# Performance work log

Hardware: AMD Instinct MI355X
Metric: run time of the kernel (lower is better)

## Reference

```python
import jax, jax.numpy as jnp
import numpy as np

NUM_ITER = 2
B, NS, NK = 64, 11, 4096
QI = KVI = QKO = VO = 128
LN_EPS = 1e-5
ATTN_EPS = 1e-8


def setup_inputs() -> dict:
    key = jax.random.key(0)
    ks = jax.random.split(key, 20)
    rn = lambda i, shp, sc: jax.random.normal(ks[i], shp, jnp.float32) * sc
    d = {
        "query": rn(0, (B, NS, QI), 1.0),
        "inputs": rn(1, (B, NK, KVI), 1.0),
        # LayerNorm params
        "ln_q_g": jnp.ones((QI,), jnp.float32),
        "ln_q_b": jnp.zeros((QI,), jnp.float32),
        "ln_kv_g": jnp.ones((KVI,), jnp.float32),
        "ln_kv_b": jnp.zeros((KVI,), jnp.float32),
        # projections (stored [in, out]; torch Linear weight transposed)
        "Wq": rn(2, (QI, QKO), QI ** -0.5),
        "Wk": rn(3, (KVI, QKO), KVI ** -0.5),
        "Wv": rn(4, (KVI, VO), KVI ** -0.5),
        # GRU cell params
        "W_ir": rn(5, (VO, VO), VO ** -0.5),
        "b_ir": jnp.zeros((VO,), jnp.float32),
        "W_iz": rn(6, (VO, VO), VO ** -0.5),
        "b_iz": jnp.zeros((VO,), jnp.float32),
        "W_hr": rn(7, (VO, VO), VO ** -0.5),
        "W_hz": rn(8, (VO, VO), VO ** -0.5),
        "W_in": rn(9, (VO, VO), VO ** -0.5),
        "b_in": jnp.zeros((VO,), jnp.float32),
        "W_hn": rn(10, (VO, VO), VO ** -0.5),
        "b_hn": jnp.zeros((VO,), jnp.float32),
    }
    return d


def _layernorm(x, g, b):
    mu = x.mean(-1, keepdims=True)
    var = ((x - mu) ** 2).mean(-1, keepdims=True)  # biased var, matches torch LN
    return (x - mu) * jax.lax.rsqrt(var + LN_EPS) * g + b


def reference(query, inputs, ln_q_g, ln_q_b, ln_kv_g, ln_kv_b, Wq, Wk, Wv,
              W_ir, b_ir, W_iz, b_iz, W_hr, W_hz, W_in, b_in, W_hn, b_hn):
    x = _layernorm(inputs, ln_kv_g, ln_kv_b)          # [b, nk, kvi]
    k = x @ Wk                                        # [b, nk, qko]
    v = x @ Wv                                        # [b, nk, vo]
    scale = 1.0 / jnp.sqrt(jnp.float32(Wq.shape[1]))
    for _ in range(NUM_ITER):
        q = _layernorm(query, ln_q_g, ln_q_b) @ Wq    # [b, ns, qko]
        q = q * scale
        # inverted SDPA: softmax over slot axis m, renormalize over key axis n
        a = jax.nn.softmax(jnp.einsum('bmc,bnc->bmn', q, k), axis=1)
        a = a / (a.sum(axis=2, keepdims=True) + ATTN_EPS)
        upd = jnp.einsum('bmn,bnc->bmc', a, v)        # [b, ns, vo]
        # GRU cell update (per-slot)
        r = jax.nn.sigmoid(upd @ W_ir + b_ir + query @ W_hr)
        z = jax.nn.sigmoid(upd @ W_iz + b_iz + query @ W_hz)
        n = jnp.tanh(upd @ W_in + b_in + r * (query @ W_hn + b_hn))
        query = (1.0 - z) * n + z * query
    return query
```

## Files before the change

kernel.cpp:

```cpp
#include <hip/hip_runtime.h>
#include <hip/hip_bf16.h>


#define NKEYS 4096

typedef short short8 __attribute__((ext_vector_type(8)));
typedef float f32x4 __attribute__((ext_vector_type(4)));

__device__ __forceinline__ unsigned short f2bf(float x) {
    unsigned u = __float_as_uint(x);
    u += 0x7fffu + ((u >> 16) & 1u);
    return (unsigned short)(u >> 16);
}

__device__ __forceinline__ int xoff(int n, int cb) {
    return n * 256 + (cb ^ ((n & 7) << 4) ^ (((n >> 3) & 3) << 5));
}

__device__ __forceinline__ void gll16(const void* g, void* l) {
    __builtin_amdgcn_global_load_lds(
        (const __attribute__((address_space(1))) unsigned int*)g,
        (__attribute__((address_space(3))) unsigned int*)l, 16, 0, 0);
}

__global__ void kqq(const float* __restrict__ query, const float* __restrict__ g,
                    const float* __restrict__ be, const float* __restrict__ Wq,
                    const float* __restrict__ Wk, char* __restrict__ qfrag) {
    int bm = blockIdx.x;
    int b = bm / 11, m = bm - b * 11;
    int c = threadIdx.x;
    __shared__ float xs[128], qs[128];
    __shared__ float red[4];
    float x = query[bm * 128 + c];
    float s = x, ss = x * x;
#pragma unroll
    for (int mask = 1; mask < 64; mask <<= 1) {
        s += __shfl_xor(s, mask);
        ss += __shfl_xor(ss, mask);
    }
    int wid = threadIdx.x >> 6;
    if ((threadIdx.x & 63) == 0) { red[wid] = s; red[2 + wid] = ss; }
    __syncthreads();
    s = red[0] + red[1]; ss = red[2] + red[3];
    float mean = s * (1.f / 128.f);
    float var = ss * (1.f / 128.f) - mean * mean;
    float rstd = rsqrtf(var + 1e-5f);
    xs[c] = (x - mean) * rstd * g[c] + be[c];
    __syncthreads();
    float acc = 0.f;
#pragma unroll 8
    for (int k = 0; k < 128; k++) acc += xs[k] * Wq[k * 128 + c];
    qs[c] = acc * 0.088388347648318447f;
    __syncthreads();
    const float4* wr = (const float4*)(Wk + c * 128);
    float qk = 0.f;
#pragma unroll 8
    for (int k4 = 0; k4 < 32; k4++) {
        float4 wv = wr[k4];
        qk += qs[k4 * 4] * wv.x + qs[k4 * 4 + 1] * wv.y +
              qs[k4 * 4 + 2] * wv.z + qs[k4 * 4 + 3] * wv.w;
    }
    int kc = c >> 5, hi = (c >> 3) & 3, j = c & 7;
    *(unsigned short*)(qfrag + b * 4096 + kc * 1024 + (hi * 16 + m) * 16 + j * 2) = f2bf(qk);
}

__global__ __launch_bounds__(256) void kf(
    const float* __restrict__ inputs, const float* __restrict__ gkv,
    const float* __restrict__ bkv, const char* __restrict__ qfrag,
    char* __restrict__ kg, float* __restrict__ yacc, float* __restrict__ dacc_g) {
    __shared__ __align__(16) char smem[18432];
    const int PO = 16384;
    int tid = threadIdx.x;
    int b = blockIdx.x >> 4, gt = blockIdx.x & 15;
    int w = tid >> 6, lane = tid & 63, hi = lane >> 4, lo = lane & 15;
    int a_ = tid >> 5, col4 = tid & 31;

    short8 qa[4];
#pragma unroll
    for (int kc = 0; kc < 4; kc++)
        qa[kc] = *(const short8*)(qfrag + b * 4096 + kc * 1024 + lane * 16);

    float4 g4  = *(const float4*)(gkv + col4 * 4);
    float4 be4 = *(const float4*)(bkv + col4 * 4);

    f32x4 y0 = {0, 0, 0, 0}, y1 = {0, 0, 0, 0};
    float dr[4] = {0, 0, 0, 0};

    const float4* inp4 = (const float4*)(inputs + ((size_t)b * NKEYS + gt * 256) * 128);

    float4 xa[8];
#pragma unroll
    for (int i = 0; i < 8; i++) xa[i] = inp4[tid + 256 * i];

#pragma unroll
    for (int t = 0; t < 4; t++) {
        float4 xb[8];
        if (t < 3) {
#pragma unroll
            for (int i = 0; i < 8; i++) xb[i] = inp4[(t + 1) * 2048 + tid + 256 * i];
        }
        size_t tb = ((size_t)(b * 64 + gt * 4 + t)) * 16384;
#pragma unroll
        for (int i = 0; i < 8; i++) {
            float4 xv = xa[i];
            int row = a_ + 8 * i;
            float s = xv.x + xv.y + xv.z + xv.w;
            float ss = xv.x * xv.x + xv.y * xv.y + xv.z * xv.z + xv.w * xv.w;
#pragma unroll
            for (int mask = 1; mask < 32; mask <<= 1) {
                s += __shfl_xor(s, mask);
                ss += __shfl_xor(ss, mask);
            }
            float mean = s * (1.f / 128.f);
            float var = ss * (1.f / 128.f) - mean * mean;
            float rstd = rsqrtf(var + 1e-5f);
            unsigned short h0 = f2bf((xv.x - mean) * rstd * g4.x + be4.x);
            unsigned short h1 = f2bf((xv.y - mean) * rstd * g4.y + be4.y);
            unsigned short h2 = f2bf((xv.z - mean) * rstd * g4.z + be4.z);
            unsigned short h3 = f2bf((xv.w - mean) * rstd * g4.w + be4.w);
            uint2 pk;
            pk.x = (unsigned)h0 | ((unsigned)h1 << 16);
            pk.y = (unsigned)h2 | ((unsigned)h3 << 16);
            int off = xoff(row, col4 * 8);
            *(uint2*)(smem + off) = pk;
            *(uint2*)(kg + tb + off) = pk;
        }
        asm volatile("s_waitcnt lgkmcnt(0)" ::: "memory");
        __builtin_amdgcn_s_barrier();
        __builtin_amdgcn_sched_barrier(0);

        f32x4 lacc = {0, 0, 0, 0};
        int n = w * 16 + lo;
#pragma unroll
        for (int kc = 0; kc < 4; kc++) {
            short8 kf8 = *(short8*)(smem + xoff(n, kc * 64 + hi * 16));
            lacc = __builtin_amdgcn_mfma_f32_16x16x32_bf16(qa[kc], kf8, lacc, 0, 0, 0);
        }
        float mx = -1e30f;
#pragma unroll
        for (int r = 0; r < 4; r++) {
            int m = hi * 4 + r;
            mx = fmaxf(mx, (m < 11) ? lacc[r] : -1e30f);
        }
        mx = fmaxf(mx, __shfl_xor(mx, 16));
        mx = fmaxf(mx, __shfl_xor(mx, 32));
        float p[4]; float s = 0.f;
#pragma unroll
        for (int r = 0; r < 4; r++) {
            int m = hi * 4 + r;
            p[r] = (m < 11) ? __expf(lacc[r] - mx) : 0.f;
            s += p[r];
        }
        s += __shfl_xor(s, 16);
        s += __shfl_xor(s, 32);
        float inv = 1.f / s;
#pragma unroll
        for (int r = 0; r < 4; r++) {
            p[r] *= inv;
            dr[r] += p[r];
            int m = hi * 4 + r;
            *(unsigned short*)(smem + PO + m * 128 + (((w * 16 + lo) * 2) ^ ((m & 7) << 4))) =
                f2bf(p[r]);
        }
        asm volatile("s_waitcnt lgkmcnt(0)" ::: "memory");
        __builtin_amdgcn_s_barrier();
        __builtin_amdgcn_sched_barrier(0);

#pragma unroll
        for (int s2 = 0; s2 < 2; s2++) {
            short8 pf = *(short8*)(smem + PO + lo * 128 + ((s2 * 64 + hi * 16) ^ ((lo & 7) << 4)));
            short8 v0, v1;
#pragma unroll
            for (int j = 0; j < 8; j++) {
                int nn = s2 * 32 + hi * 8 + j;
                v0[j] = *(short*)(smem + xoff(nn, (w * 32 + lo) * 2));
                v1[j] = *(short*)(smem + xoff(nn, (w * 32 + 16 + lo) * 2));
            }
            y0 = __builtin_amdgcn_mfma_f32_16x16x32_bf16(pf, v0, y0, 0, 0, 0);
            y1 = __builtin_amdgcn_mfma_f32_16x16x32_bf16(pf, v1, y1, 0, 0, 0);
        }
        asm volatile("s_waitcnt lgkmcnt(0)" ::: "memory");
        __builtin_amdgcn_s_barrier();
        __builtin_amdgcn_sched_barrier(0);
        if (t < 3) {
#pragma unroll
            for (int i = 0; i < 8; i++) xa[i] = xb[i];
        }
    }

#pragma unroll
    for (int r = 0; r < 4; r++) {
        int m = hi * 4 + r;
        if (m < 11) {
            atomicAdd(&yacc[(b * 16 + m) * 128 + w * 32 + lo], y0[r]);
            atomicAdd(&yacc[(b * 16 + m) * 128 + w * 32 + 16 + lo], y1[r]);
        }
    }
#pragma unroll
    for (int mask = 1; mask < 16; mask <<= 1) {
#pragma unroll
        for (int r = 0; r < 4; r++) dr[r] += __shfl_xor(dr[r], mask);
    }
    if (lo == 0) {
#pragma unroll
        for (int r = 0; r < 4; r++) {
            int m = hi * 4 + r;
            if (m < 11) atomicAdd(&dacc_g[b * 16 + m], dr[r]);
        }
    }
}

__global__ __launch_bounds__(256) void kb(
    const char* __restrict__ kg, const char* __restrict__ qfrag,
    float* __restrict__ yacc, float* __restrict__ dacc_g) {
    __shared__ __align__(16) char smem[34816];
    const int PO = 32768;
    int tid = threadIdx.x;
    int b = blockIdx.x >> 4, gt = blockIdx.x & 15;
    int w = tid >> 6, lane = tid & 63, hi = lane >> 4, lo = lane & 15;

    short8 qa[4];
#pragma unroll
    for (int kc = 0; kc < 4; kc++)
        qa[kc] = *(const short8*)(qfrag + b * 4096 + kc * 1024 + lane * 16);

    f32x4 y0 = {0, 0, 0, 0}, y1 = {0, 0, 0, 0};
    float dr[4] = {0, 0, 0, 0};

    size_t base = ((size_t)(b * 64 + gt * 4)) * 16384;
    int reg = w * 4096;

#pragma unroll
    for (int j = 0; j < 4; j++) {
        int o = reg + j * 1024;
        gll16(kg + base + o + lane * 16, smem + o);
    }

#pragma unroll
    for (int t = 0; t < 4; t++) {
        int XB = (t & 1) * 16384;
        if (t < 3) {
            size_t tbn = base + (size_t)(t + 1) * 16384;
            int nb = ((t + 1) & 1) * 16384;
#pragma unroll
            for (int j = 0; j < 4; j++) {
                int o = reg + j * 1024;
                gll16(kg + tbn + o + lane * 16, smem + nb + o);
            }
            asm volatile("s_waitcnt vmcnt(4)" ::: "memory");
        } else {
            asm volatile("s_waitcnt vmcnt(0)" ::: "memory");
        }
        __builtin_amdgcn_s_barrier();
        __builtin_amdgcn_sched_barrier(0);

        f32x4 lacc = {0, 0, 0, 0};
        int n = w * 16 + lo;
#pragma unroll
        for (int kc = 0; kc < 4; kc++) {
            short8 kf8 = *(short8*)(smem + XB + xoff(n, kc * 64 + hi * 16));
            lacc = __builtin_amdgcn_mfma_f32_16x16x32_bf16(qa[kc], kf8, lacc, 0, 0, 0);
        }
        float mx = -1e30f;
#pragma unroll
        for (int r = 0; r < 4; r++) {
            int m = hi * 4 + r;
            mx = fmaxf(mx, (m < 11) ? lacc[r] : -1e30f);
        }
        mx = fmaxf(mx, __shfl_xor(mx, 16));
        mx = fmaxf(mx, __shfl_xor(mx, 32));
        float p[4]; float s = 0.f;
#pragma unroll
        for (int r = 0; r < 4; r++) {
            int m = hi * 4 + r;
            p[r] = (m < 11) ? __expf(lacc[r] - mx) : 0.f;
            s += p[r];
        }
        s += __shfl_xor(s, 16);
        s += __shfl_xor(s, 32);
        float inv = 1.f / s;
#pragma unroll
        for (int r = 0; r < 4; r++) {
            p[r] *= inv;
            dr[r] += p[r];
            int m = hi * 4 + r;
            *(unsigned short*)(smem + PO + m * 128 + (((w * 16 + lo) * 2) ^ ((m & 7) << 4))) =
                f2bf(p[r]);
        }
        asm volatile("s_waitcnt lgkmcnt(0)" ::: "memory");
        __builtin_amdgcn_s_barrier();
        __builtin_amdgcn_sched_barrier(0);

#pragma unroll
        for (int s2 = 0; s2 < 2; s2++) {
            short8 pf = *(short8*)(smem + PO + lo * 128 + ((s2 * 64 + hi * 16) ^ ((lo & 7) << 4)));
            short8 v0, v1;
#pragma unroll
            for (int j = 0; j < 8; j++) {
                int nn = s2 * 32 + hi * 8 + j;
                v0[j] = *(short*)(smem + XB + xoff(nn, (w * 32 + lo) * 2));
                v1[j] = *(short*)(smem + XB + xoff(nn, (w * 32 + 16 + lo) * 2));
            }
            y0 = __builtin_amdgcn_mfma_f32_16x16x32_bf16(pf, v0, y0, 0, 0, 0);
            y1 = __builtin_amdgcn_mfma_f32_16x16x32_bf16(pf, v1, y1, 0, 0, 0);
        }
        asm volatile("s_waitcnt lgkmcnt(0)" ::: "memory");
        __builtin_amdgcn_s_barrier();
        __builtin_amdgcn_sched_barrier(0);
    }

#pragma unroll
    for (int r = 0; r < 4; r++) {
        int m = hi * 4 + r;
        if (m < 11) {
            atomicAdd(&yacc[(b * 16 + m) * 128 + w * 32 + lo], y0[r]);
            atomicAdd(&yacc[(b * 16 + m) * 128 + w * 32 + 16 + lo], y1[r]);
        }
    }
#pragma unroll
    for (int mask = 1; mask < 16; mask <<= 1) {
#pragma unroll
        for (int r = 0; r < 4; r++) dr[r] += __shfl_xor(dr[r], mask);
    }
    if (lo == 0) {
#pragma unroll
        for (int r = 0; r < 4; r++) {
            int m = hi * 4 + r;
            if (m < 11) atomicAdd(&dacc_g[b * 16 + m], dr[r]);
        }
    }
}

__global__ void kun(const float* __restrict__ yacc, const float* __restrict__ dacc,
                    const float* __restrict__ qcur, const float* __restrict__ Wv,
                    const float* __restrict__ W_ir, const float* __restrict__ b_ir,
                    const float* __restrict__ W_iz, const float* __restrict__ b_iz,
                    const float* __restrict__ W_hr, const float* __restrict__ W_hz,
                    const float* __restrict__ W_in, const float* __restrict__ b_in,
                    const float* __restrict__ W_hn, const float* __restrict__ b_hn,
                    float* __restrict__ qnext) {
    int bm = blockIdx.x;
    int b = bm / 11, m = bm % 11;
    int c = threadIdx.x;
    __shared__ float ys[128], us[128], qs[128];
    float den = dacc[b * 16 + m] + 1e-8f;
    ys[c] = yacc[(b * 16 + m) * 128 + c] / den;
    qs[c] = qcur[bm * 128 + c];
    __syncthreads();
    float upd = 0.f;
#pragma unroll 4
    for (int k = 0; k < 128; k++) upd += ys[k] * Wv[k * 128 + c];
    us[c] = upd;
    __syncthreads();
    float air = 0, aiz = 0, ain = 0, ahr = 0, ahz = 0, ahn = 0;
#pragma unroll 4
    for (int k = 0; k < 128; k++) {
        float u = us[k], q = qs[k];
        air += u * W_ir[k * 128 + c];
        aiz += u * W_iz[k * 128 + c];
        ain += u * W_in[k * 128 + c];
        ahr += q * W_hr[k * 128 + c];
        ahz += q * W_hz[k * 128 + c];
        ahn += q * W_hn[k * 128 + c];
    }
    float r = 1.f / (1.f + expf(-(air + b_ir[c] + ahr)));
    float z = 1.f / (1.f + expf(-(aiz + b_iz[c] + ahz)));
    float n = tanhf(ain + b_in[c] + r * (ahn + b_hn[c]));
    qnext[bm * 128 + c] = (1.f - z) * n + z * qs[c];
}

__global__ void kq(const float* __restrict__ query, const float* __restrict__ g,
                   const float* __restrict__ be, const float* __restrict__ Wq,
                   float* __restrict__ qout) {
    int bm = blockIdx.x;
    int c = threadIdx.x;
    __shared__ float xs[128];
    __shared__ float red[4];
    float x = query[bm * 128 + c];
    float s = x, ss = x * x;
#pragma unroll
    for (int mask = 1; mask < 64; mask <<= 1) {
        s += __shfl_xor(s, mask);
        ss += __shfl_xor(ss, mask);
    }
    int wid = threadIdx.x >> 6;
    if ((threadIdx.x & 63) == 0) { red[wid] = s; red[2 + wid] = ss; }
    __syncthreads();
    s = red[0] + red[1]; ss = red[2] + red[3];
    float mean = s * (1.f / 128.f);
    float var = ss * (1.f / 128.f) - mean * mean;
    float rstd = rsqrtf(var + 1e-5f);
    xs[c] = (x - mean) * rstd * g[c] + be[c];
    __syncthreads();
    float acc = 0.f;
#pragma unroll 8
    for (int k = 0; k < 128; k++) acc += xs[k] * Wq[k * 128 + c];
    qout[bm * 128 + c] = acc * 0.088388347648318447f;
}

__global__ __launch_bounds__(256) void ks(
    const float* __restrict__ inputs, const float* __restrict__ gkv,
    const float* __restrict__ bkv, const float* __restrict__ Wk,
    const float* __restrict__ Wv, const float* __restrict__ qbuf,
    float* __restrict__ upd_acc, float* __restrict__ d_acc) {
    __shared__ __align__(16) char smem[51200];
    const int XO = 0, KO = 16384, VB = 32768, PO = 49152;

    int tid = threadIdx.x;
    int b = blockIdx.x >> 4, g = blockIdx.x & 15;
    int w = tid >> 6, lane = tid & 63, hi = lane >> 4, lo = lane & 15;

    short8 bk[2][4], bv[2][4];
#pragma unroll
    for (int ct = 0; ct < 2; ct++) {
        int col = w * 32 + ct * 16 + lo;
#pragma unroll
        for (int kc = 0; kc < 4; kc++) {
            short8 fk, fv;
#pragma unroll
            for (int j = 0; j < 8; j++) {
                int rr = kc * 32 + hi * 8 + j;
                fk[j] = (short)f2bf(Wk[rr * 128 + col]);
                fv[j] = (short)f2bf(Wv[rr * 128 + col]);
            }
            bk[ct][kc] = fk; bv[ct][kc] = fv;
        }
    }
    short8 qa[4];
#pragma unroll
    for (int kc = 0; kc < 4; kc++) {
        short8 f;
#pragma unroll
        for (int j = 0; j < 8; j++)
            f[j] = (lo < 11) ? (short)f2bf(qbuf[(b * 11 + lo) * 128 + kc * 32 + hi * 8 + j])
                             : (short)0;
        qa[kc] = f;
    }
    int col4 = tid & 31;
    float4 g4  = *(const float4*)(gkv + col4 * 4);
    float4 be4 = *(const float4*)(bkv + col4 * 4);

    f32x4 uacc0 = {0, 0, 0, 0}, uacc1 = {0, 0, 0, 0};
    float dacc[4] = {0, 0, 0, 0};

    const float4* inp4 = (const float4*)(inputs + ((size_t)b * NKEYS + g * 256) * 128);
    int a_ = tid >> 5;

    for (int t = 0; t < 4; t++) {
#pragma unroll
        for (int i = 0; i < 8; i++) {
            int f = tid + 256 * i;
            float4 xv = inp4[t * 2048 + f];
            int row = a_ + 8 * i;
            float s = xv.x + xv.y + xv.z + xv.w;
            float ss = xv.x * xv.x + xv.y * xv.y + xv.z * xv.z + xv.w * xv.w;
#pragma unroll
            for (int mask = 1; mask < 32; mask <<= 1) {
                s += __shfl_xor(s, mask);
                ss += __shfl_xor(ss, mask);
            }
            float mean = s * (1.f / 128.f);
            float var = ss * (1.f / 128.f) - mean * mean;
            float rstd = rsqrtf(var + 1e-5f);
            unsigned short h0 = f2bf((xv.x - mean) * rstd * g4.x + be4.x);
            unsigned short h1 = f2bf((xv.y - mean) * rstd * g4.y + be4.y);
            unsigned short h2 = f2bf((xv.z - mean) * rstd * g4.z + be4.z);
            unsigned short h3 = f2bf((xv.w - mean) * rstd * g4.w + be4.w);
            uint2 pk;
            pk.x = (unsigned)h0 | ((unsigned)h1 << 16);
            pk.y = (unsigned)h2 | ((unsigned)h3 << 16);
            int byte = row * 256 + ((col4 * 8) ^ ((row & 7) << 4));
            *(uint2*)(smem + XO + byte) = pk;
        }
        __syncthreads();
#pragma unroll
        for (int mt = 0; mt < 4; mt++) {
            f32x4 ka0 = {0,0,0,0}, ka1 = {0,0,0,0}, va0 = {0,0,0,0}, va1 = {0,0,0,0};
            int arow = mt * 16 + lo;
#pragma unroll
            for (int kc = 0; kc < 4; kc++) {
                int abyte = arow * 256 + ((kc * 64 + hi * 16) ^ ((arow & 7) << 4));
                short8 af = *(short8*)(smem + XO + abyte);
                ka0 = __builtin_amdgcn_mfma_f32_16x16x32_bf16(af, bk[0][kc], ka0, 0, 0, 0);
                ka1 = __builtin_amdgcn_mfma_f32_16x16x32_bf16(af, bk[1][kc], ka1, 0, 0, 0);
                va0 = __builtin_amdgcn_mfma_f32_16x16x32_bf16(af, bv[0][kc], va0, 0, 0, 0);
                va1 = __builtin_amdgcn_mfma_f32_16x16x32_bf16(af, bv[1][kc], va1, 0, 0, 0);
            }
#pragma unroll
            for (int r = 0; r < 4; r++) {
                int n = mt * 16 + hi * 4 + r;
                int c0 = w * 32 + lo;
                int c1 = c0 + 16;
                *(unsigned short*)(smem + KO + n * 256 + ((c0 * 2) ^ ((n & 7) << 4))) = f2bf(ka0[r]);
                *(unsigned short*)(smem + KO + n * 256 + ((c1 * 2) ^ ((n & 7) << 4))) = f2bf(ka1[r]);
                *(unsigned short*)(smem + VB + c0 * 128 + ((n * 2) ^ ((c0 & 7) << 4))) = f2bf(va0[r]);
                *(unsigned short*)(smem + VB + c1 * 128 + ((n * 2) ^ ((c1 & 7) << 4))) = f2bf(va1[r]);
            }
        }
        __syncthreads();
        {
            f32x4 lacc = {0, 0, 0, 0};
            int n = w * 16 + lo;
#pragma unroll
            for (int kc = 0; kc < 4; kc++) {
                int kbyte = n * 256 + ((kc * 64 + hi * 16) ^ ((n & 7) << 4));
                short8 kf8 = *(short8*)(smem + KO + kbyte);
                lacc = __builtin_amdgcn_mfma_f32_16x16x32_bf16(qa[kc], kf8, lacc, 0, 0, 0);
            }
            float mx = -1e30f;
#pragma unroll
            for (int r = 0; r < 4; r++) {
                int m = hi * 4 + r;
                float v = (m < 11) ? lacc[r] : -1e30f;
                mx = fmaxf(mx, v);
            }
            mx = fmaxf(mx, __shfl_xor(mx, 16));
            mx = fmaxf(mx, __shfl_xor(mx, 32));
            float p[4]; float s = 0.f;
#pragma unroll
            for (int r = 0; r < 4; r++) {
                int m = hi * 4 + r;
                p[r] = (m < 11) ? __expf(lacc[r] - mx) : 0.f;
                s += p[r];
            }
            s += __shfl_xor(s, 16);
            s += __shfl_xor(s, 32);
            float inv = 1.f / s;
#pragma unroll
            for (int r = 0; r < 4; r++) {
                p[r] *= inv;
                dacc[r] += p[r];
                int m = hi * 4 + r;
                *(unsigned short*)(smem + PO + m * 128 + (((w * 16 + lo) * 2) ^ ((m & 7) << 4))) =
                    f2bf(p[r]);
            }
        }
        __syncthreads();
#pragma unroll
        for (int kc2 = 0; kc2 < 2; kc2++) {
            int pbyte = lo * 128 + ((kc2 * 64 + hi * 16) ^ ((lo & 7) << 4));
            short8 pf = *(short8*)(smem + PO + pbyte);
            int c0 = w * 32 + lo;
            int vb0 = c0 * 128 + ((kc2 * 64 + hi * 16) ^ ((c0 & 7) << 4));
            short8 vf0 = *(short8*)(smem + VB + vb0);
            uacc0 = __builtin_amdgcn_mfma_f32_16x16x32_bf16(pf, vf0, uacc0, 0, 0, 0);
            int c1 = c0 + 16;
            int vb1 = c1 * 128 + ((kc2 * 64 + hi * 16) ^ ((c1 & 7) << 4));
            short8 vf1 = *(short8*)(smem + VB + vb1);
            uacc1 = __builtin_amdgcn_mfma_f32_16x16x32_bf16(pf, vf1, uacc1, 0, 0, 0);
        }
    }
#pragma unroll
    for (int r = 0; r < 4; r++) {
        int m = hi * 4 + r;
        if (m < 11) {
            atomicAdd(&upd_acc[(b * 16 + m) * 128 + w * 32 + lo], uacc0[r]);
            atomicAdd(&upd_acc[(b * 16 + m) * 128 + w * 32 + 16 + lo], uacc1[r]);
        }
    }
#pragma unroll
    for (int mask = 1; mask < 16; mask <<= 1) {
#pragma unroll
        for (int r = 0; r < 4; r++) dacc[r] += __shfl_xor(dacc[r], mask);
    }
    if (lo == 0) {
#pragma unroll
        for (int r = 0; r < 4; r++) {
            int m = hi * 4 + r;
            if (m < 11) atomicAdd(&d_acc[b * 16 + m], dacc[r]);
        }
    }
}

__global__ void ku(const float* __restrict__ upd_acc, const float* __restrict__ d_acc,
                   const float* __restrict__ qcur,
                   const float* __restrict__ W_ir, const float* __restrict__ b_ir,
                   const float* __restrict__ W_iz, const float* __restrict__ b_iz,
                   const float* __restrict__ W_hr, const float* __restrict__ W_hz,
                   const float* __restrict__ W_in, const float* __restrict__ b_in,
                   const float* __restrict__ W_hn, const float* __restrict__ b_hn,
                   float* __restrict__ qnext) {
    int bm = blockIdx.x;
    int b = bm / 11, m = bm % 11;
    int c = threadIdx.x;
    __shared__ float us[128], qs[128];
    float den = d_acc[b * 16 + m] + 1e-8f;
    us[c] = upd_acc[(b * 16 + m) * 128 + c] / den;
    qs[c] = qcur[bm * 128 + c];
    __syncthreads();
    float air = 0, aiz = 0, ain = 0, ahr = 0, ahz = 0, ahn = 0;
#pragma unroll 4
    for (int k = 0; k < 128; k++) {
        float u = us[k], q = qs[k];
        air += u * W_ir[k * 128 + c];
        aiz += u * W_iz[k * 128 + c];
        ain += u * W_in[k * 128 + c];
        ahr += q * W_hr[k * 128 + c];
        ahz += q * W_hz[k * 128 + c];
        ahn += q * W_hn[k * 128 + c];
    }
    float r = 1.f / (1.f + expf(-(air + b_ir[c] + ahr)));
    float z = 1.f / (1.f + expf(-(aiz + b_iz[c] + ahz)));
    float n = tanhf(ain + b_in[c] + r * (ahn + b_hn[c]));
    qnext[bm * 128 + c] = (1.f - z) * n + z * qs[c];
}

extern "C" void kernel_launch(void* const* d_in, const int* in_sizes, int n_in,
                              void* d_out, int out_size, void* d_ws, size_t ws_size,
                              hipStream_t stream) {
    const float* query   = (const float*)d_in[0];
    const float* inputs  = (const float*)d_in[1];
    const float* ln_q_g  = (const float*)d_in[2];
    const float* ln_q_b  = (const float*)d_in[3];
    const float* ln_kv_g = (const float*)d_in[4];
    const float* ln_kv_b = (const float*)d_in[5];
    const float* Wq      = (const float*)d_in[6];
    const float* Wk      = (const float*)d_in[7];
    const float* Wv      = (const float*)d_in[8];
    const float* W_ir    = (const float*)d_in[9];
    const float* b_ir    = (const float*)d_in[10];
    const float* W_iz    = (const float*)d_in[11];
    const float* b_iz    = (const float*)d_in[12];
    const float* W_hr    = (const float*)d_in[13];
    const float* W_hz    = (const float*)d_in[14];
    const float* W_in    = (const float*)d_in[15];
    const float* b_in    = (const float*)d_in[16];
    const float* W_hn    = (const float*)d_in[17];
    const float* b_hn    = (const float*)d_in[18];

    char* ws = (char*)d_ws;
    float* query_buf = (float*)(ws);
    float* yacc      = (float*)(ws + 360448);
    float* dacc      = (float*)(ws + 884736);
    char*  qfrag     = ws + 888832;
    char*  kg        = ws + 1150976;
    const size_t need = 1150976ull + 67108864ull;

    if (ws_size >= need) {
        hipMemsetAsync(ws + 360448, 0, 790528, stream);
        kqq<<<704, 128, 0, stream>>>(query, ln_q_g, ln_q_b, Wq, Wk, qfrag);
        kf<<<1024, 256, 0, stream>>>(inputs, ln_kv_g, ln_kv_b, qfrag, kg, yacc, dacc);
        kun<<<704, 128, 0, stream>>>(yacc, dacc, query, Wv,
                                     W_ir, b_ir, W_iz, b_iz, W_hr, W_hz,
                                     W_in, b_in, W_hn, b_hn, query_buf);
        hipMemsetAsync(ws + 360448, 0, 790528, stream);
        kqq<<<704, 128, 0, stream>>>(query_buf, ln_q_g, ln_q_b, Wq, Wk, qfrag);
        kb<<<1024, 256, 0, stream>>>(kg, qfrag, yacc, dacc);
        kun<<<704, 128, 0, stream>>>(yacc, dacc, query_buf, Wv,
                                     W_ir, b_ir, W_iz, b_iz, W_hr, W_hz,
                                     W_in, b_in, W_hn, b_hn, (float*)d_out);
    } else {
        float* q_buf = (float*)(ws + 888832);
        const float* cur = query;
        for (int it = 0; it < 2; it++) {
            kq<<<704, 128, 0, stream>>>(cur, ln_q_g, ln_q_b, Wq, q_buf);
            hipMemsetAsync(ws + 360448, 0, 524288 + 4096, stream);
            ks<<<1024, 256, 0, stream>>>(inputs, ln_kv_g, ln_kv_b, Wk, Wv, q_buf, yacc, dacc);
            float* qn = (it == 0) ? query_buf : (float*)d_out;
            ku<<<704, 128, 0, stream>>>(yacc, dacc, cur,
                                        W_ir, b_ir, W_iz, b_iz, W_hr, W_hz,
                                        W_in, b_in, W_hn, b_hn, qn);
            cur = query_buf;
        }
    }
}
```

Baseline: 155.2 us.

## Split first-pass key kernel into more blocks with per-thread 16-column LayerNorm rows

The first attention kernel now launches 2048 blocks, each covering 128 keys in two tiles, instead of 1024 blocks covering 256 keys in four tiles. Each thread loads 16 contiguous floats of a row, so the LayerNorm reduction needs only three shuffles and the bf16 results are stored as 16-byte writes. The next tile is loaded after the current one is normalized rather than double-buffered. The memsets also shrink to cover only the accumulators, since the query fragments are fully overwritten. This trades more atomics and less in-block prefetch for more parallelism and cheaper reductions.

```diff
diff --git a/kernel.cpp b/kernel.cpp
--- a/kernel.cpp
+++ b/kernel.cpp
@@ -71,59 +71,79 @@
     __shared__ __align__(16) char smem[18432];
     const int PO = 16384;
     int tid = threadIdx.x;
-    int b = blockIdx.x >> 4, gt = blockIdx.x & 15;
+    int bb = blockIdx.x >> 5, gt = blockIdx.x & 31;
     int w = tid >> 6, lane = tid & 63, hi = lane >> 4, lo = lane & 15;
-    int a_ = tid >> 5, col4 = tid & 31;
+    int r0 = tid >> 3, rj = tid & 7;
 
     short8 qa[4];
 #pragma unroll
     for (int kc = 0; kc < 4; kc++)
-        qa[kc] = *(const short8*)(qfrag + b * 4096 + kc * 1024 + lane * 16);
-
-    float4 g4  = *(const float4*)(gkv + col4 * 4);
-    float4 be4 = *(const float4*)(bkv + col4 * 4);
+        qa[kc] = *(const short8*)(qfrag + bb * 4096 + kc * 1024 + lane * 16);
+
+    float4 gx[4], bx[4];
+#pragma unroll
+    for (int i = 0; i < 4; i++) {
+        gx[i] = *(const float4*)(gkv + rj * 16 + i * 4);
+        bx[i] = *(const float4*)(bkv + rj * 16 + i * 4);
+    }
 
     f32x4 y0 = {0, 0, 0, 0}, y1 = {0, 0, 0, 0};
     float dr[4] = {0, 0, 0, 0};
 
-    const float4* inp4 = (const float4*)(inputs + ((size_t)b * NKEYS + gt * 256) * 128);
-
-    float4 xa[8];
-#pragma unroll
-    for (int i = 0; i < 8; i++) xa[i] = inp4[tid + 256 * i];
-
-#pragma unroll
-    for (int t = 0; t < 4; t++) {
-        float4 xb[8];
-        if (t < 3) {
-#pragma unroll
-            for (int i = 0; i < 8; i++) xb[i] = inp4[(t + 1) * 2048 + tid + 256 * i];
-        }
-        size_t tb = ((size_t)(b * 64 + gt * 4 + t)) * 16384;
-#pragma unroll
-        for (int i = 0; i < 8; i++) {
-            float4 xv = xa[i];
-            int row = a_ + 8 * i;
-            float s = xv.x + xv.y + xv.z + xv.w;
-            float ss = xv.x * xv.x + xv.y * xv.y + xv.z * xv.z + xv.w * xv.w;
-#pragma unroll
-            for (int mask = 1; mask < 32; mask <<= 1) {
-                s += __shfl_xor(s, mask);
-                ss += __shfl_xor(ss, mask);
-            }
+    const float* xbase = inputs + ((size_t)bb * NKEYS + gt * 128) * 128;
+
+    float4 xa[2][4];
+#pragma unroll
+    for (int p = 0; p < 2; p++)
+#pragma unroll
+        for (int i = 0; i < 4; i++)
+            xa[p][i] = *(const float4*)(xbase + (r0 + p * 32) * 128 + rj * 16 + i * 4);
+
+#pragma unroll
+    for (int t = 0; t < 2; t++) {
+        size_t tb = ((size_t)(bb * 64 + gt * 2 + t)) * 16384;
+#pragma unroll
+        for (int p = 0; p < 2; p++) {
+            int row = r0 + p * 32;
+            float s = 0.f, ss = 0.f;
+#pragma unroll
+            for (int i = 0; i < 4; i++) {
+                float4 v = xa[p][i];
+                s += v.x + v.y + v.z + v.w;
+                ss += v.x * v.x + v.y * v.y + v.z * v.z + v.w * v.w;
+            }
+            s += __shfl_xor(s, 1); ss += __shfl_xor(ss, 1);
+            s += __shfl_xor(s, 2); ss += __shfl_xor(ss, 2);
+            s += __shfl_xor(s, 4); ss += __shfl_xor(ss, 4);
             float mean = s * (1.f / 128.f);
             float var = ss * (1.f / 128.f) - mean * mean;
             float rstd = rsqrtf(var + 1e-5f);
-            unsigned short h0 = f2bf((xv.x - mean) * rstd * g4.x + be4.x);
-            unsigned short h1 = f2bf((xv.y - mean) * rstd * g4.y + be4.y);
-            unsigned short h2 = f2bf((xv.z - mean) * rstd * g4.z + be4.z);
-            unsigned short h3 = f2bf((xv.w - mean) * rstd * g4.w + be4.w);
-            uint2 pk;
-            pk.x = (unsigned)h0 | ((unsigned)h1 << 16);
-            pk.y = (unsigned)h2 | ((unsigned)h3 << 16);
-            int off = xoff(row, col4 * 8);
-            *(uint2*)(smem + off) = pk;
-            *(uint2*)(kg + tb + off) = pk;
+            unsigned u[8];
+#pragma unroll
+            for (int i = 0; i < 4; i++) {
+                float4 v = xa[p][i];
+                unsigned short h0 = f2bf((v.x - mean) * rstd * gx[i].x + bx[i].x);
+                unsigned short h1 = f2bf((v.y - mean) * rstd * gx[i].y + bx[i].y);
+                unsigned short h2 = f2bf((v.z - mean) * rstd * gx[i].z + bx[i].z);
+                unsigned short h3 = f2bf((v.w - mean) * rstd * gx[i].w + bx[i].w);
+                u[2 * i]     = (unsigned)h0 | ((unsigned)h1 << 16);
+                u[2 * i + 1] = (unsigned)h2 | ((unsigned)h3 << 16);
+            }
+            uint4 q0 = {u[0], u[1], u[2], u[3]};
+            uint4 q1 = {u[4], u[5], u[6], u[7]};
+            int off0 = xoff(row, rj * 32);
+            int off1 = xoff(row, rj * 32 + 16);
+            *(uint4*)(smem + off0) = q0;
+            *(uint4*)(smem + off1) = q1;
+            *(uint4*)(kg + tb + off0) = q0;
+            *(uint4*)(kg + tb + off1) = q1;
+        }
+        if (t == 0) {
+#pragma unroll
+            for (int p = 0; p < 2; p++)
+#pragma unroll
+                for (int i = 0; i < 4; i++)
+                    xa[p][i] = *(const float4*)(xbase + (64 + r0 + p * 32) * 128 + rj * 16 + i * 4);
         }
         asm volatile("s_waitcnt lgkmcnt(0)" ::: "memory");
         __builtin_amdgcn_s_barrier();
@@ -182,18 +202,14 @@
         asm volatile("s_waitcnt lgkmcnt(0)" ::: "memory");
         __builtin_amdgcn_s_barrier();
         __builtin_amdgcn_sched_barrier(0);
-        if (t < 3) {
-#pragma unroll
-            for (int i = 0; i < 8; i++) xa[i] = xb[i];
-        }
     }
 
 #pragma unroll
     for (int r = 0; r < 4; r++) {
         int m = hi * 4 + r;
         if (m < 11) {
-            atomicAdd(&yacc[(b * 16 + m) * 128 + w * 32 + lo], y0[r]);
-            atomicAdd(&yacc[(b * 16 + m) * 128 + w * 32 + 16 + lo], y1[r]);
+            atomicAdd(&yacc[(bb * 16 + m) * 128 + w * 32 + lo], y0[r]);
+            atomicAdd(&yacc[(bb * 16 + m) * 128 + w * 32 + 16 + lo], y1[r]);
         }
     }
 #pragma unroll
@@ -205,7 +221,7 @@
 #pragma unroll
         for (int r = 0; r < 4; r++) {
             int m = hi * 4 + r;
-            if (m < 11) atomicAdd(&dacc_g[b * 16 + m], dr[r]);
+            if (m < 11) atomicAdd(&dacc_g[bb * 16 + m], dr[r]);
         }
     }
 }
@@ -637,13 +653,13 @@
     const size_t need = 1150976ull + 67108864ull;
 
     if (ws_size >= need) {
-        hipMemsetAsync(ws + 360448, 0, 790528, stream);
+        hipMemsetAsync(ws + 360448, 0, 528384, stream);
         kqq<<<704, 128, 0, stream>>>(query, ln_q_g, ln_q_b, Wq, Wk, qfrag);
-        kf<<<1024, 256, 0, stream>>>(inputs, ln_kv_g, ln_kv_b, qfrag, kg, yacc, dacc);
+        kf<<<2048, 256, 0, stream>>>(inputs, ln_kv_g, ln_kv_b, qfrag, kg, yacc, dacc);
         kun<<<704, 128, 0, stream>>>(yacc, dacc, query, Wv,
                                      W_ir, b_ir, W_iz, b_iz, W_hr, W_hz,
                                      W_in, b_in, W_hn, b_hn, query_buf);
-        hipMemsetAsync(ws + 360448, 0, 790528, stream);
+        hipMemsetAsync(ws + 360448, 0, 528384, stream);
         kqq<<<704, 128, 0, stream>>>(query_buf, ln_q_g, ln_q_b, Wq, Wk, qfrag);
         kb<<<1024, 256, 0, stream>>>(kg, qfrag, yacc, dacc);
         kun<<<704, 128, 0, stream>>>(yacc, dacc, query_buf, Wv,
```

Result: slower. 176.9 us (+13.9%).

## Fuse accumulator zeroing and next-iteration query projection into GRU kernel

Applied to the files above, without the earlier changes.

Drops both hipMemsetAsync calls. Each block of the query-projection and GRU kernels now zeroes its own accumulator row. The second standalone query-projection launch is folded into the first GRU kernel, which in mode 1 computes LayerNorm, Wq, scale and Wk-folding and writes the bf16 query fragments. This cuts launch and memset overhead. Separately, the bulk kernel's double-buffer loop now waits for all loads and syncs at the top of each step before issuing the prefetch, dropping the trailing barrier, which may reduce load/compute overlap.

```diff
diff --git a/kernel.cpp b/kernel.cpp
--- a/kernel.cpp
+++ b/kernel.cpp
@@ -25,10 +25,13 @@
 
 __global__ void kqq(const float* __restrict__ query, const float* __restrict__ g,
                     const float* __restrict__ be, const float* __restrict__ Wq,
-                    const float* __restrict__ Wk, char* __restrict__ qfrag) {
+                    const float* __restrict__ Wk, char* __restrict__ qfrag,
+                    float* __restrict__ yz, float* __restrict__ dz) {
     int bm = blockIdx.x;
     int b = bm / 11, m = bm - b * 11;
     int c = threadIdx.x;
+    yz[(b * 16 + m) * 128 + c] = 0.f;
+    if (c == 0) dz[b * 16 + m] = 0.f;
     __shared__ float xs[128], qs[128];
     __shared__ float red[4];
     float x = query[bm * 128 + c];
@@ -239,6 +242,9 @@
 #pragma unroll
     for (int t = 0; t < 4; t++) {
         int XB = (t & 1) * 16384;
+        asm volatile("s_waitcnt vmcnt(0)" ::: "memory");
+        __builtin_amdgcn_s_barrier();
+        __builtin_amdgcn_sched_barrier(0);
         if (t < 3) {
             size_t tbn = base + (size_t)(t + 1) * 16384;
             int nb = ((t + 1) & 1) * 16384;
@@ -247,12 +253,7 @@
                 int o = reg + j * 1024;
                 gll16(kg + tbn + o + lane * 16, smem + nb + o);
             }
-            asm volatile("s_waitcnt vmcnt(4)" ::: "memory");
-        } else {
-            asm volatile("s_waitcnt vmcnt(0)" ::: "memory");
-        }
-        __builtin_amdgcn_s_barrier();
-        __builtin_amdgcn_sched_barrier(0);
+        }
 
         f32x4 lacc = {0, 0, 0, 0};
         int n = w * 16 + lo;
@@ -305,7 +306,6 @@
             y1 = __builtin_amdgcn_mfma_f32_16x16x32_bf16(pf, v1, y1, 0, 0, 0);
         }
         asm volatile("s_waitcnt lgkmcnt(0)" ::: "memory");
-        __builtin_amdgcn_s_barrier();
         __builtin_amdgcn_sched_barrier(0);
     }
 
@@ -338,11 +338,16 @@
                     const float* __restrict__ W_hr, const float* __restrict__ W_hz,
                     const float* __restrict__ W_in, const float* __restrict__ b_in,
                     const float* __restrict__ W_hn, const float* __restrict__ b_hn,
-                    float* __restrict__ qnext) {
+                    float* __restrict__ qnext, int mode,
+                    const float* __restrict__ lqg, const float* __restrict__ lqb,
+                    const float* __restrict__ Wq, const float* __restrict__ Wk,
+                    char* __restrict__ qfrag, float* __restrict__ yz,
+                    float* __restrict__ dz) {
     int bm = blockIdx.x;
     int b = bm / 11, m = bm % 11;
     int c = threadIdx.x;
     __shared__ float ys[128], us[128], qs[128];
+    __shared__ float red[4];
     float den = dacc[b * 16 + m] + 1e-8f;
     ys[c] = yacc[(b * 16 + m) * 128 + c] / den;
     qs[c] = qcur[bm * 128 + c];
@@ -366,7 +371,41 @@
     float r = 1.f / (1.f + expf(-(air + b_ir[c] + ahr)));
     float z = 1.f / (1.f + expf(-(aiz + b_iz[c] + ahz)));
     float n = tanhf(ain + b_in[c] + r * (ahn + b_hn[c]));
-    qnext[bm * 128 + c] = (1.f - z) * n + z * qs[c];
+    float qn = (1.f - z) * n + z * qs[c];
+    qnext[bm * 128 + c] = qn;
+    if (mode == 0) return;
+    yz[(b * 16 + m) * 128 + c] = 0.f;
+    if (c == 0) dz[b * 16 + m] = 0.f;
+    float s = qn, ss = qn * qn;
+#pragma unroll
+    for (int mask = 1; mask < 64; mask <<= 1) {
+        s += __shfl_xor(s, mask);
+        ss += __shfl_xor(ss, mask);
+    }
+    int wid = c >> 6;
+    if ((c & 63) == 0) { red[wid] = s; red[2 + wid] = ss; }
+    __syncthreads();
+    s = red[0] + red[1]; ss = red[2] + red[3];
+    float mean = s * (1.f / 128.f);
+    float var = ss * (1.f / 128.f) - mean * mean;
+    float rstd = rsqrtf(var + 1e-5f);
+    ys[c] = (qn - mean) * rstd * lqg[c] + lqb[c];
+    __syncthreads();
+    float acc = 0.f;
+#pragma unroll 8
+    for (int k = 0; k < 128; k++) acc += ys[k] * Wq[k * 128 + c];
+    us[c] = acc * 0.088388347648318447f;
+    __syncthreads();
+    const float4* wr = (const float4*)(Wk + c * 128);
+    float qk = 0.f;
+#pragma unroll 8
+    for (int k4 = 0; k4 < 32; k4++) {
+        float4 wv = wr[k4];
+        qk += us[k4 * 4] * wv.x + us[k4 * 4 + 1] * wv.y +
+              us[k4 * 4 + 2] * wv.z + us[k4 * 4 + 3] * wv.w;
+    }
+    int kc = c >> 5, hi = (c >> 3) & 3, j = c & 7;
+    *(unsigned short*)(qfrag + b * 4096 + kc * 1024 + (hi * 16 + m) * 16 + j * 2) = f2bf(qk);
 }
 
 __global__ void kq(const float* __restrict__ query, const float* __restrict__ g,
@@ -637,18 +676,17 @@
     const size_t need = 1150976ull + 67108864ull;
 
     if (ws_size >= need) {
-        hipMemsetAsync(ws + 360448, 0, 790528, stream);
-        kqq<<<704, 128, 0, stream>>>(query, ln_q_g, ln_q_b, Wq, Wk, qfrag);
+        kqq<<<704, 128, 0, stream>>>(query, ln_q_g, ln_q_b, Wq, Wk, qfrag, yacc, dacc);
         kf<<<1024, 256, 0, stream>>>(inputs, ln_kv_g, ln_kv_b, qfrag, kg, yacc, dacc);
         kun<<<704, 128, 0, stream>>>(yacc, dacc, query, Wv,
                                      W_ir, b_ir, W_iz, b_iz, W_hr, W_hz,
-                                     W_in, b_in, W_hn, b_hn, query_buf);
-        hipMemsetAsync(ws + 360448, 0, 790528, stream);
-        kqq<<<704, 128, 0, stream>>>(query_buf, ln_q_g, ln_q_b, Wq, Wk, qfrag);
+                                     W_in, b_in, W_hn, b_hn, query_buf, 1,
+                                     ln_q_g, ln_q_b, Wq, Wk, qfrag, yacc, dacc);
         kb<<<1024, 256, 0, stream>>>(kg, qfrag, yacc, dacc);
         kun<<<704, 128, 0, stream>>>(yacc, dacc, query_buf, Wv,
                                      W_ir, b_ir, W_iz, b_iz, W_hr, W_hz,
-                                     W_in, b_in, W_hn, b_hn, (float*)d_out);
+                                     W_in, b_in, W_hn, b_hn, (float*)d_out, 0,
+                                     ln_q_g, ln_q_b, Wq, Wk, qfrag, yacc, dacc);
     } else {
         float* q_buf = (float*)(ws + 888832);
         const float* cur = query;
```

New measurement: 145.0 us. -6.6%, faster.
